# Performance work log

Hardware: AMD Instinct MI355X
Metric: run time of the kernel (lower is better)

## Reference

```python
import jax, jax.numpy as jnp
import numpy as np

N_NODES = 100000


def setup_inputs() -> dict:
    key = jax.random.key(0)
    k1, k2, k3, k4, k5 = jax.random.split(key, 5)
    feature = jax.random.normal(k1, (N_NODES, 64), dtype=jnp.float32)
    src = jax.random.randint(k2, (1600000,), 0, N_NODES, dtype=jnp.int64)
    dst = jax.random.randint(k3, (1600000,), 0, N_NODES, dtype=jnp.int64)
    W = jax.random.normal(k4, (64, 64), dtype=jnp.float32) * 0.1  # [in_feats, out_feats]
    b = jax.random.normal(k5, (64,), dtype=jnp.float32) * 0.1
    return {"feature": feature, "src": src, "dst": dst, "W": W, "b": b}


def reference(feature, src, dst, W, b):
    # message: m_e = h[src_e]; reduce: mean over mailbox per dst node.
    msgs = feature[src]                                   # [E, d] gather
    summed = jax.ops.segment_sum(msgs, dst, num_segments=N_NODES)  # [N, d]
    ones = jnp.ones((dst.shape[0],), dtype=feature.dtype)
    deg = jax.ops.segment_sum(ones, dst, num_segments=N_NODES)    # [N]
    mean = summed / jnp.maximum(deg, 1.0)[:, None]
    # DGL: nodes with no incoming messages keep their original feature
    h = jnp.where((deg > 0)[:, None], mean, feature)
    # apply_nodes: ReLU(W h + b)
    out = jax.nn.relu(h @ W + b)
    return out
```

## Files before the change

### kernel.cpp

```cpp
#include <hip/hip_runtime.h>
#include <hip/hip_bf16.h>

#define D 64
#define LOGB 7
#define BNODES 128
#define GRP6 32
#define CH6 1024
#define SUBN 32
#define CHUNK 1024
#define TN 64

__device__ __forceinline__ float blo(unsigned u) { return __uint_as_float(u << 16); }
__device__ __forceinline__ float bhi(unsigned u) { return __uint_as_float(u & 0xffff0000u); }
__device__ __forceinline__ ushort f2bfr(float x) {
    __hip_bfloat16 hb = __float2bfloat16(x);
    return *reinterpret_cast<ushort*>(&hb);
}


__global__ __launch_bounds__(256) void k_transform5(
    const float* __restrict__ feat, const float* __restrict__ W,
    ushort* __restrict__ g, int n_nodes,
    const int* __restrict__ dst, int n_edges,
    int* __restrict__ bcnt, int nbkt, int hb)
{
    __shared__ float ft[D][TN];
    __shared__ float Ws[D][D];
    __shared__ int sc[1024];

    int t = threadIdx.x;
    int n0 = blockIdx.x * TN;

    if (blockIdx.x == 0 && t < 64) g[(size_t)n_nodes * D + t] = 0;

    {
        const float4* W4 = (const float4*)W;
        float4* Ws4 = (float4*)&Ws[0][0];
        #pragma unroll
        for (int i = 0; i < 4; ++i) Ws4[t + i * 256] = W4[t + i * 256];
    }
    {
        const float4* f4 = (const float4*)feat;
        #pragma unroll
        for (int it = 0; it < 4; ++it) {
            int i = it * 256 + t;
            int r = i >> 4, c = i & 15;
            int node = n0 + r;
            float4 v = (node < n_nodes) ? f4[(size_t)node * 16 + c]
                                        : make_float4(0.f, 0.f, 0.f, 0.f);
            ft[4 * c + 0][r] = v.x;
            ft[4 * c + 1][r] = v.y;
            ft[4 * c + 2][r] = v.z;
            ft[4 * c + 3][r] = v.w;
        }
    }
    __syncthreads();

    int nq = t >> 4, cq = t & 15;
    int n4 = nq * 4, c4 = cq * 4;

    float4 a0 = make_float4(0.f, 0.f, 0.f, 0.f);
    float4 a1 = a0, a2 = a0, a3 = a0;

    #pragma unroll 16
    for (int k = 0; k < D; ++k) {
        float4 fv = *reinterpret_cast<const float4*>(&ft[k][n4]);
        float4 wv = *reinterpret_cast<const float4*>(&Ws[k][c4]);
        a0.x = fmaf(fv.x, wv.x, a0.x); a0.y = fmaf(fv.x, wv.y, a0.y);
        a0.z = fmaf(fv.x, wv.z, a0.z); a0.w = fmaf(fv.x, wv.w, a0.w);
        a1.x = fmaf(fv.y, wv.x, a1.x); a1.y = fmaf(fv.y, wv.y, a1.y);
        a1.z = fmaf(fv.y, wv.z, a1.z); a1.w = fmaf(fv.y, wv.w, a1.w);
        a2.x = fmaf(fv.z, wv.x, a2.x); a2.y = fmaf(fv.z, wv.y, a2.y);
        a2.z = fmaf(fv.z, wv.z, a2.z); a2.w = fmaf(fv.z, wv.w, a2.w);
        a3.x = fmaf(fv.w, wv.x, a3.x); a3.y = fmaf(fv.w, wv.y, a3.y);
        a3.z = fmaf(fv.w, wv.z, a3.z); a3.w = fmaf(fv.w, wv.w, a3.w);
    }

    float4 accs[4] = {a0, a1, a2, a3};
    #pragma unroll
    for (int i = 0; i < 4; ++i) {
        int node = n0 + n4 + i;
        if (node < n_nodes) {
            ushort4 o;
            o.x = f2bfr(accs[i].x);
            o.y = f2bfr(accs[i].y);
            o.z = f2bfr(accs[i].z);
            o.w = f2bfr(accs[i].w);
            *reinterpret_cast<ushort4*>(g + (size_t)node * D + c4) = o;
        }
    }

    if (blockIdx.x < (unsigned)hb) {
        for (int i = t; i < 1024; i += 256) sc[i] = 0;
        __syncthreads();
        int n4e = n_edges >> 2;
        const int4* d4 = (const int4*)dst;
        int base = blockIdx.x * 4096;
        #pragma unroll
        for (int k2 = 0; k2 < 16; ++k2) {
            int i = base + k2 * 256 + t;
            if (i < n4e) {
                int4 d = d4[i];
                atomicAdd(&sc[d.x >> LOGB], 1);
                atomicAdd(&sc[d.y >> LOGB], 1);
                atomicAdd(&sc[d.z >> LOGB], 1);
                atomicAdd(&sc[d.w >> LOGB], 1);
            }
        }
        if (blockIdx.x == 0 && t == 0)
            for (int e = n4e << 2; e < n_edges; ++e)
                atomicAdd(&bcnt[dst[e] >> LOGB], 1);
        __syncthreads();
        for (int i = t; i < nbkt; i += 256) {
            int c = sc[i];
            if (c) atomicAdd(&bcnt[i], c);
        }
    }
}


__global__ __launch_bounds__(256) void k_bin_count(
    const int* __restrict__ dst, int* __restrict__ cnt, int n_edges, int nbkt)
{
    __shared__ int sc[1024];
    int t = threadIdx.x;
    for (int i = t; i < 1024; i += 256) sc[i] = 0;
    __syncthreads();
    int n4 = n_edges >> 2;
    const int4* d4 = (const int4*)dst;
    int stride = gridDim.x * 256;
    for (int i = blockIdx.x * 256 + t; i < n4; i += stride) {
        int4 d = d4[i];
        atomicAdd(&sc[d.x >> LOGB], 1);
        atomicAdd(&sc[d.y >> LOGB], 1);
        atomicAdd(&sc[d.z >> LOGB], 1);
        atomicAdd(&sc[d.w >> LOGB], 1);
    }
    if (blockIdx.x == 0 && t == 0)
        for (int e = n4 << 2; e < n_edges; ++e) atomicAdd(&cnt[dst[e] >> LOGB], 1);
    __syncthreads();
    for (int i = t; i < nbkt; i += 256) {
        int c = sc[i];
        if (c) atomicAdd(&cnt[i], c);
    }
}

__global__ __launch_bounds__(1024) void k_bin_scan(
    const int* __restrict__ cnt, int* __restrict__ base,
    int* __restrict__ cursor, int nbkt)
{
    int t = threadIdx.x;
    int v = (t < nbkt) ? cnt[t] : 0;
    int lane = t & 63;
    int incl = v;
    #pragma unroll
    for (int o = 1; o < 64; o <<= 1) {
        int u = __shfl_up(incl, o, 64);
        if (lane >= o) incl += u;
    }
    __shared__ int wtot[16];
    if (lane == 63) wtot[t >> 6] = incl;
    __syncthreads();
    int wpre = 0;
    int w = t >> 6;
    for (int i = 0; i < w; ++i) wpre += wtot[i];
    int excl = wpre + incl - v;
    if (t < nbkt) { base[t] = excl; cursor[t] = excl; }
    if (t == nbkt - 1) base[nbkt] = excl + v;
}

__global__ __launch_bounds__(256) void k_bin_scatter(
    const int* __restrict__ src, const int* __restrict__ dst,
    int* __restrict__ cursor, unsigned* __restrict__ packed,
    int n_edges, int sbits)
{
    __shared__ int s_cnt[1024];
    __shared__ int s_base[1024];
    __shared__ int s_gb[1024];
    __shared__ int wtot[4];
    __shared__ unsigned s_stage[4096];
    __shared__ int s_addr[4096];

    int t = threadIdx.x;
    int chbase = blockIdx.x * 4096;
    int count = n_edges - chbase;
    if (count > 4096) count = 4096;

    for (int i = t; i < 1024; i += 256) s_cnt[i] = 0;
    __syncthreads();

    #pragma unroll
    for (int k = 0; k < 16; ++k) {
        int i = t + k * 256;
        if (i < count) atomicAdd(&s_cnt[dst[chbase + i] >> LOGB], 1);
    }
    __syncthreads();

    int b4 = t * 4;
    int v0 = s_cnt[b4], v1 = s_cnt[b4 + 1], v2 = s_cnt[b4 + 2], v3 = s_cnt[b4 + 3];
    int ssum = v0 + v1 + v2 + v3;
    int lane = t & 63;
    int incl = ssum;
    #pragma unroll
    for (int o = 1; o < 64; o <<= 1) {
        int u = __shfl_up(incl, o, 64);
        if (lane >= o) incl += u;
    }
    if (lane == 63) wtot[t >> 6] = incl;
    __syncthreads();
    int wpre = 0;
    int w = t >> 6;
    for (int i = 0; i < w; ++i) wpre += wtot[i];
    int excl = wpre + incl - ssum;
    s_base[b4]     = excl;
    s_base[b4 + 1] = excl + v0;
    s_base[b4 + 2] = excl + v0 + v1;
    s_base[b4 + 3] = excl + v0 + v1 + v2;
    __syncthreads();

    for (int i = t; i < 1024; i += 256) {
        int c = s_cnt[i];
        s_gb[i] = c ? atomicAdd(&cursor[i], c) : 0;
    }
    __syncthreads();
    for (int i = t; i < 1024; i += 256) s_cnt[i] = s_base[i];
    __syncthreads();

    #pragma unroll
    for (int k = 0; k < 16; ++k) {
        int i = t + k * 256;
        if (i < count) {
            int e = chbase + i;
            int d = dst[e];
            int s = src[e];
            int bkt = d >> LOGB;
            int pos = atomicAdd(&s_cnt[bkt], 1);
            s_stage[pos] = ((unsigned)(d & (BNODES - 1)) << sbits) | (unsigned)s;
            s_addr[pos]  = s_gb[bkt] + (pos - s_base[bkt]);
        }
    }
    __syncthreads();

    #pragma unroll
    for (int k = 0; k < 16; ++k) {
        int i = t + k * 256;
        if (i < count) packed[s_addr[i]] = s_stage[i];
    }
}


__global__ __launch_bounds__(256) void k_sort128(
    const unsigned* __restrict__ packed,
    const int* __restrict__ bbase,
    int* __restrict__ csr2,
    int* __restrict__ noff,
    int n_nodes, int sbits)
{
    __shared__ int s_cnt[BNODES];
    __shared__ int s_off[BNODES + 1];

    int t = threadIdx.x;
    int b = blockIdx.x;
    int gb = bbase[b], cnt = bbase[b + 1] - gb;

    if (t < BNODES) s_cnt[t] = 0;
    __syncthreads();
    for (int i = t; i < cnt; i += 256)
        atomicAdd(&s_cnt[packed[gb + i] >> sbits], 1);
    __syncthreads();

    if (t < 64) {
        int v0 = s_cnt[2 * t], v1 = s_cnt[2 * t + 1];
        int s = v0 + v1, incl = s;
        #pragma unroll
        for (int o = 1; o < 64; o <<= 1) {
            int u = __shfl_up(incl, o, 64);
            if (t >= o) incl += u;
        }
        int excl = incl - s;
        s_off[2 * t] = excl;
        s_off[2 * t + 1] = excl + v0;
        if (t == 63) s_off[BNODES] = incl;
    }
    __syncthreads();

    if (t <= BNODES) {
        int node = b * BNODES + t;
        if (node <= n_nodes) noff[node] = gb + s_off[t];
    }
    if (t < BNODES) s_cnt[t] = s_off[t];
    __syncthreads();

    unsigned smask = (1u << sbits) - 1u;
    for (int i = t; i < cnt; i += 256) {
        unsigned v = packed[gb + i];
        int pos = atomicAdd(&s_cnt[v >> sbits], 1);
        csr2[gb + pos] = (int)(v & smask);
    }
}


__global__ __launch_bounds__(256) void k_bucket6(
    const ushort* __restrict__ g,
    const float* __restrict__ bias,
    const int* __restrict__ noff,
    const int* __restrict__ csr2,
    float* __restrict__ out, int n_nodes)
{
    __shared__ int s_src[CH6];
    __shared__ int s_noff[GRP6 + 1];

    int t = threadIdx.x;
    int n0 = blockIdx.x * GRP6;
    if (t <= GRP6) {
        int node = n0 + t;
        s_noff[t] = noff[node > n_nodes ? n_nodes : node];
    }
    __syncthreads();

    int lane = t & 63, wid = t >> 6;
    int q = lane >> 4;
    int m = lane & 15;
    const ushort* gm = g + 4 * m;

    float4 acc[8];
    #pragma unroll
    for (int k = 0; k < 8; ++k) acc[k] = make_float4(0.f, 0.f, 0.f, 0.f);

    int beg = s_noff[0], end = s_noff[GRP6];
    for (int cb = beg; cb < end; cb += CH6) {
        int ce = cb + CH6 < end ? cb + CH6 : end;
        __syncthreads();
        for (int i = cb + t; i < ce; i += 256) s_src[i - cb] = csr2[i];
        __syncthreads();

        #pragma unroll
        for (int k = 0; k < 8; ++k) {
            int r = wid * 8 + k;
            int lo = s_noff[r], hi = s_noff[r + 1];
            if (lo < cb) lo = cb;
            if (hi > ce) hi = ce;
            float4 a = acc[k];
            for (int i = lo; i < hi; i += 16) {
                int i0 = i + q, i1 = i0 + 4, i2 = i0 + 8, i3 = i0 + 12;
                int s0 = (i0 < hi) ? s_src[i0 - cb] : n_nodes;
                int s1 = (i1 < hi) ? s_src[i1 - cb] : n_nodes;
                int s2 = (i2 < hi) ? s_src[i2 - cb] : n_nodes;
                int s3 = (i3 < hi) ? s_src[i3 - cb] : n_nodes;
                uint2 u0 = *reinterpret_cast<const uint2*>(gm + (size_t)s0 * D);
                uint2 u1 = *reinterpret_cast<const uint2*>(gm + (size_t)s1 * D);
                uint2 u2 = *reinterpret_cast<const uint2*>(gm + (size_t)s2 * D);
                uint2 u3 = *reinterpret_cast<const uint2*>(gm + (size_t)s3 * D);
                a.x += blo(u0.x); a.y += bhi(u0.x); a.z += blo(u0.y); a.w += bhi(u0.y);
                a.x += blo(u1.x); a.y += bhi(u1.x); a.z += blo(u1.y); a.w += bhi(u1.y);
                a.x += blo(u2.x); a.y += bhi(u2.x); a.z += blo(u2.y); a.w += bhi(u2.y);
                a.x += blo(u3.x); a.y += bhi(u3.x); a.z += blo(u3.y); a.w += bhi(u3.y);
            }
            acc[k] = a;
        }
    }

    float4 bj = *reinterpret_cast<const float4*>(bias + 4 * m);
    #pragma unroll
    for (int k = 0; k < 8; ++k) {
        float4 v = acc[k];
        v.x += __shfl_xor(v.x, 16, 64);
        v.y += __shfl_xor(v.y, 16, 64);
        v.z += __shfl_xor(v.z, 16, 64);
        v.w += __shfl_xor(v.w, 16, 64);
        v.x += __shfl_xor(v.x, 32, 64);
        v.y += __shfl_xor(v.y, 32, 64);
        v.z += __shfl_xor(v.z, 32, 64);
        v.w += __shfl_xor(v.w, 32, 64);
        if ((k & 3) == q) {
            int r = wid * 8 + k;
            int node = n0 + r;
            if (node < n_nodes) {
                int dgt = s_noff[r + 1] - s_noff[r];
                float4 res;
                if (dgt > 0) {
                    float inv = 1.0f / (float)dgt;
                    res = make_float4(v.x * inv, v.y * inv, v.z * inv, v.w * inv);
                } else {
                    uint2 u = *reinterpret_cast<const uint2*>(gm + (size_t)node * D);
                    res = make_float4(blo(u.x), bhi(u.x), blo(u.y), bhi(u.y));
                }
                res.x = fmaxf(res.x + bj.x, 0.0f);
                res.y = fmaxf(res.y + bj.y, 0.0f);
                res.z = fmaxf(res.z + bj.z, 0.0f);
                res.w = fmaxf(res.w + bj.w, 0.0f);
                *reinterpret_cast<float4*>(out + (size_t)node * D + 4 * m) = res;
            }
        }
    }
}


__global__ __launch_bounds__(256) void k_bucket4(
    const ushort* __restrict__ g,
    const float* __restrict__ bias,
    const int* __restrict__ base,
    const unsigned* __restrict__ packed,
    float* __restrict__ out,
    int n_nodes, int sbits)
{
    __shared__ unsigned s_raw[CHUNK];
    __shared__ unsigned s_rec[CHUNK];
    __shared__ int s_cnt[SUBN];
    __shared__ int s_off[SUBN + 1];

    int t = threadIdx.x;
    int lane = t & 63;
    int wid  = t >> 6;
    int q = lane >> 4;
    int m = lane & 15;
    int bkt = blockIdx.x >> 2;
    int sub = blockIdx.x & 3;
    int gb = base[bkt], ge = base[bkt + 1];
    unsigned smask = (1u << sbits) - 1u;
    const ushort* gm = g + 4 * m;

    float4 acc[8];
    int degv[8];
    #pragma unroll
    for (int k = 0; k < 8; ++k) {
        acc[k] = make_float4(0.f, 0.f, 0.f, 0.f);
        degv[k] = 0;
    }

    for (int cb = gb; cb < ge; cb += CHUNK) {
        int cnt = ge - cb;
        if (cnt > CHUNK) cnt = CHUNK;
        __syncthreads();
        if (t < SUBN) s_cnt[t] = 0;
        for (int i = t; i < cnt; i += 256) s_raw[i] = packed[cb + i];
        __syncthreads();
        for (int i = t; i < cnt; i += 256) {
            unsigned key = s_raw[i] >> sbits;
            if ((int)(key >> 5) == sub) atomicAdd(&s_cnt[key & 31], 1);
        }
        __syncthreads();
        if (t < 32) {
            int v = s_cnt[t];
            int incl = v;
            #pragma unroll
            for (int o = 1; o < 32; o <<= 1) {
                int u = __shfl_up(incl, o, 64);
                if (t >= o) incl += u;
            }
            int excl = incl - v;
            s_off[t] = excl;
            s_cnt[t] = excl;
            if (t == 31) s_off[32] = incl;
        }
        __syncthreads();
        for (int i = t; i < cnt; i += 256) {
            unsigned v = s_raw[i];
            unsigned key = v >> sbits;
            if ((int)(key >> 5) == sub) {
                int pos = atomicAdd(&s_cnt[key & 31], 1);
                s_rec[pos] = v;
            }
        }
        __syncthreads();
        #pragma unroll
        for (int k = 0; k < 8; ++k) {
            int r = wid * 8 + k;
            int beg = s_off[r], end = s_off[r + 1];
            float4 a = acc[k];
            for (int i = beg; i < end; i += 16) {
                int i0 = i + q, i1 = i0 + 4, i2 = i0 + 8, i3 = i0 + 12;
                bool p0 = i0 < end, p1 = i1 < end, p2 = i2 < end, p3 = i3 < end;
                unsigned r0 = s_rec[p0 ? i0 : beg];
                unsigned r1 = s_rec[p1 ? i1 : beg];
                unsigned r2 = s_rec[p2 ? i2 : beg];
                unsigned r3 = s_rec[p3 ? i3 : beg];
                int s0 = (int)(r0 & smask), s1 = (int)(r1 & smask);
                int s2 = (int)(r2 & smask), s3 = (int)(r3 & smask);
                uint2 u0 = *reinterpret_cast<const uint2*>(gm + (size_t)s0 * D);
                uint2 u1 = *reinterpret_cast<const uint2*>(gm + (size_t)s1 * D);
                uint2 u2 = *reinterpret_cast<const uint2*>(gm + (size_t)s2 * D);
                uint2 u3 = *reinterpret_cast<const uint2*>(gm + (size_t)s3 * D);
                a.x += p0 ? blo(u0.x) : 0.0f;  a.y += p0 ? bhi(u0.x) : 0.0f;
                a.z += p0 ? blo(u0.y) : 0.0f;  a.w += p0 ? bhi(u0.y) : 0.0f;
                a.x += p1 ? blo(u1.x) : 0.0f;  a.y += p1 ? bhi(u1.x) : 0.0f;
                a.z += p1 ? blo(u1.y) : 0.0f;  a.w += p1 ? bhi(u1.y) : 0.0f;
                a.x += p2 ? blo(u2.x) : 0.0f;  a.y += p2 ? bhi(u2.x) : 0.0f;
                a.z += p2 ? blo(u2.y) : 0.0f;  a.w += p2 ? bhi(u2.y) : 0.0f;
                a.x += p3 ? blo(u3.x) : 0.0f;  a.y += p3 ? bhi(u3.x) : 0.0f;
                a.z += p3 ? blo(u3.y) : 0.0f;  a.w += p3 ? bhi(u3.y) : 0.0f;
            }
            acc[k] = a;
            degv[k] += end - beg;
        }
    }

    float4 bj = *reinterpret_cast<const float4*>(bias + 4 * m);
    int n0 = (bkt << LOGB) + sub * SUBN;
    #pragma unroll
    for (int k = 0; k < 8; ++k) {
        float4 v = acc[k];
        v.x += __shfl_xor(v.x, 16, 64);
        v.y += __shfl_xor(v.y, 16, 64);
        v.z += __shfl_xor(v.z, 16, 64);
        v.w += __shfl_xor(v.w, 16, 64);
        v.x += __shfl_xor(v.x, 32, 64);
        v.y += __shfl_xor(v.y, 32, 64);
        v.z += __shfl_xor(v.z, 32, 64);
        v.w += __shfl_xor(v.w, 32, 64);
        if ((k & 3) == q) {
            int node = n0 + wid * 8 + k;
            if (node < n_nodes) {
                int dgt = degv[k];
                float4 res;
                if (dgt > 0) {
                    float inv = 1.0f / (float)dgt;
                    res = make_float4(v.x * inv, v.y * inv, v.z * inv, v.w * inv);
                } else {
                    uint2 u = *reinterpret_cast<const uint2*>(gm + (size_t)node * D);
                    res = make_float4(blo(u.x), bhi(u.x), blo(u.y), bhi(u.y));
                }
                res.x = fmaxf(res.x + bj.x, 0.0f);
                res.y = fmaxf(res.y + bj.y, 0.0f);
                res.z = fmaxf(res.z + bj.z, 0.0f);
                res.w = fmaxf(res.w + bj.w, 0.0f);
                *reinterpret_cast<float4*>(out + (size_t)node * D + 4 * m) = res;
            }
        }
    }
}


extern "C" void kernel_launch(void* const* d_in, const int* in_sizes, int n_in,
                              void* d_out, int out_size, void* d_ws, size_t ws_size,
                              hipStream_t stream)
{
    const float* feat = (const float*)d_in[0];
    const int*   src  = (const int*)d_in[1];
    const int*   dst  = (const int*)d_in[2];
    const float* W    = (const float*)d_in[3];
    const float* b    = (const float*)d_in[4];
    float* out = (float*)d_out;

    int n_nodes = in_sizes[0] / D;
    int n_edges = in_sizes[1];
    int nbkt = (n_nodes + BNODES - 1) >> LOGB;

    int sbits = 1;
    while ((1 << sbits) < n_nodes && sbits < 25) sbits++;

    size_t base_off   = 0;
    size_t cnt_off    = (((size_t)(nbkt + 1) * 4) + 63) & ~(size_t)63;
    size_t cursor_off = (cnt_off + (size_t)nbkt * 4 + 63) & ~(size_t)63;
    size_t noff_off   = (cursor_off + (size_t)nbkt * 4 + 63) & ~(size_t)63;
    size_t packed_off = (noff_off + ((size_t)n_nodes + 1) * 4 + 63) & ~(size_t)63;
    size_t csr2_off   = (packed_off + (size_t)n_edges * 4 + 63) & ~(size_t)63;
    size_t g_off      = (csr2_off + (size_t)n_edges * 4 + 63) & ~(size_t)63;
    size_t need_new   = g_off + ((size_t)n_nodes + 1) * D * 2;

    size_t o_packed_off = noff_off;
    size_t o_g_off      = (o_packed_off + (size_t)n_edges * 4 + 63) & ~(size_t)63;
    size_t need_old     = o_g_off + ((size_t)n_nodes + 1) * D * 2;

    bool common_ok = (nbkt <= 1024) && (sbits + LOGB <= 32) &&
                     ((1 << sbits) >= n_nodes);
    char* ws = (char*)d_ws;
    int tblk = (n_nodes + TN - 1) / TN;
    int nblk = (n_edges + 4095) / 4096;
    int hb = ((n_edges >> 2) + 4095) / 4096;
    bool fuse_hist = (hb <= tblk);

    if (common_ok && ws_size >= need_new) {
        int* bbase   = (int*)(ws + base_off);
        int* bcnt    = (int*)(ws + cnt_off);
        int* bcursor = (int*)(ws + cursor_off);
        int* noff    = (int*)(ws + noff_off);
        unsigned* packed = (unsigned*)(ws + packed_off);
        int* csr2    = (int*)(ws + csr2_off);
        ushort* g    = (ushort*)(ws + g_off);

        hipMemsetAsync(bcnt, 0, (size_t)nbkt * 4, stream);
        k_transform5<<<tblk, 256, 0, stream>>>(feat, W, g, n_nodes, dst, n_edges,
                                               bcnt, nbkt, fuse_hist ? hb : 0);
        if (!fuse_hist)
            k_bin_count<<<512, 256, 0, stream>>>(dst, bcnt, n_edges, nbkt);
        k_bin_scan<<<1, 1024, 0, stream>>>(bcnt, bbase, bcursor, nbkt);
        k_bin_scatter<<<nblk, 256, 0, stream>>>(src, dst, bcursor, packed,
                                                n_edges, sbits);
        k_sort128<<<nbkt, 256, 0, stream>>>(packed, bbase, csr2, noff,
                                            n_nodes, sbits);
        int ngrp6 = (n_nodes + GRP6 - 1) / GRP6;
        k_bucket6<<<ngrp6, 256, 0, stream>>>(g, b, noff, csr2, out, n_nodes);
    } else if (common_ok && ws_size >= need_old) {
        int* bbase   = (int*)(ws + base_off);
        int* bcnt    = (int*)(ws + cnt_off);
        int* bcursor = (int*)(ws + cursor_off);
        unsigned* packed = (unsigned*)(ws + o_packed_off);
        ushort* g    = (ushort*)(ws + o_g_off);

        hipMemsetAsync(bcnt, 0, (size_t)nbkt * 4, stream);
        k_transform5<<<tblk, 256, 0, stream>>>(feat, W, g, n_nodes, dst, n_edges,
                                               bcnt, nbkt, fuse_hist ? hb : 0);
        if (!fuse_hist)
            k_bin_count<<<512, 256, 0, stream>>>(dst, bcnt, n_edges, nbkt);
        k_bin_scan<<<1, 1024, 0, stream>>>(bcnt, bbase, bcursor, nbkt);
        k_bin_scatter<<<nblk, 256, 0, stream>>>(src, dst, bcursor, packed,
                                                n_edges, sbits);
        k_bucket4<<<nbkt * 4, 256, 0, stream>>>(g, b, bbase, packed, out,
                                                n_nodes, sbits);
    }
}
```

Baseline: 101.1 us.

## Move feature transform into scatter kernel and run histogram standalone

The histogram is split out of the transform kernel into a standalone k_hist launch with 256 blocks. The dense feature transform (h@W to bf16) now shares one launch with the bin scatter, with block ranges picking which path runs, so the GEMM blocks overlap the scatter's atomic-heavy work. The unused fallback k_bucket4 path is dropped, and the function returns early if workspace is too small. Using shared memory as a union of both paths' layouts raises per-block LDS use to about 45 KB, which may lower occupancy for the transform blocks.

```diff
diff --git a/kernel.cpp b/kernel.cpp
--- a/kernel.cpp
+++ b/kernel.cpp
@@ -6,8 +6,6 @@
 #define BNODES 128
 #define GRP6 32
 #define CH6 1024
-#define SUBN 32
-#define CHUNK 1024
 #define TN 64
 
 __device__ __forceinline__ float blo(unsigned u) { return __uint_as_float(u << 16); }
@@ -18,108 +16,7 @@
 }
 
 
-__global__ __launch_bounds__(256) void k_transform5(
-    const float* __restrict__ feat, const float* __restrict__ W,
-    ushort* __restrict__ g, int n_nodes,
-    const int* __restrict__ dst, int n_edges,
-    int* __restrict__ bcnt, int nbkt, int hb)
-{
-    __shared__ float ft[D][TN];
-    __shared__ float Ws[D][D];
-    __shared__ int sc[1024];
-
-    int t = threadIdx.x;
-    int n0 = blockIdx.x * TN;
-
-    if (blockIdx.x == 0 && t < 64) g[(size_t)n_nodes * D + t] = 0;
-
-    {
-        const float4* W4 = (const float4*)W;
-        float4* Ws4 = (float4*)&Ws[0][0];
-        #pragma unroll
-        for (int i = 0; i < 4; ++i) Ws4[t + i * 256] = W4[t + i * 256];
-    }
-    {
-        const float4* f4 = (const float4*)feat;
-        #pragma unroll
-        for (int it = 0; it < 4; ++it) {
-            int i = it * 256 + t;
-            int r = i >> 4, c = i & 15;
-            int node = n0 + r;
-            float4 v = (node < n_nodes) ? f4[(size_t)node * 16 + c]
-                                        : make_float4(0.f, 0.f, 0.f, 0.f);
-            ft[4 * c + 0][r] = v.x;
-            ft[4 * c + 1][r] = v.y;
-            ft[4 * c + 2][r] = v.z;
-            ft[4 * c + 3][r] = v.w;
-        }
-    }
-    __syncthreads();
-
-    int nq = t >> 4, cq = t & 15;
-    int n4 = nq * 4, c4 = cq * 4;
-
-    float4 a0 = make_float4(0.f, 0.f, 0.f, 0.f);
-    float4 a1 = a0, a2 = a0, a3 = a0;
-
-    #pragma unroll 16
-    for (int k = 0; k < D; ++k) {
-        float4 fv = *reinterpret_cast<const float4*>(&ft[k][n4]);
-        float4 wv = *reinterpret_cast<const float4*>(&Ws[k][c4]);
-        a0.x = fmaf(fv.x, wv.x, a0.x); a0.y = fmaf(fv.x, wv.y, a0.y);
-        a0.z = fmaf(fv.x, wv.z, a0.z); a0.w = fmaf(fv.x, wv.w, a0.w);
-        a1.x = fmaf(fv.y, wv.x, a1.x); a1.y = fmaf(fv.y, wv.y, a1.y);
-        a1.z = fmaf(fv.y, wv.z, a1.z); a1.w = fmaf(fv.y, wv.w, a1.w);
-        a2.x = fmaf(fv.z, wv.x, a2.x); a2.y = fmaf(fv.z, wv.y, a2.y);
-        a2.z = fmaf(fv.z, wv.z, a2.z); a2.w = fmaf(fv.z, wv.w, a2.w);
-        a3.x = fmaf(fv.w, wv.x, a3.x); a3.y = fmaf(fv.w, wv.y, a3.y);
-        a3.z = fmaf(fv.w, wv.z, a3.z); a3.w = fmaf(fv.w, wv.w, a3.w);
-    }
-
-    float4 accs[4] = {a0, a1, a2, a3};
-    #pragma unroll
-    for (int i = 0; i < 4; ++i) {
-        int node = n0 + n4 + i;
-        if (node < n_nodes) {
-            ushort4 o;
-            o.x = f2bfr(accs[i].x);
-            o.y = f2bfr(accs[i].y);
-            o.z = f2bfr(accs[i].z);
-            o.w = f2bfr(accs[i].w);
-            *reinterpret_cast<ushort4*>(g + (size_t)node * D + c4) = o;
-        }
-    }
-
-    if (blockIdx.x < (unsigned)hb) {
-        for (int i = t; i < 1024; i += 256) sc[i] = 0;
-        __syncthreads();
-        int n4e = n_edges >> 2;
-        const int4* d4 = (const int4*)dst;
-        int base = blockIdx.x * 4096;
-        #pragma unroll
-        for (int k2 = 0; k2 < 16; ++k2) {
-            int i = base + k2 * 256 + t;
-            if (i < n4e) {
-                int4 d = d4[i];
-                atomicAdd(&sc[d.x >> LOGB], 1);
-                atomicAdd(&sc[d.y >> LOGB], 1);
-                atomicAdd(&sc[d.z >> LOGB], 1);
-                atomicAdd(&sc[d.w >> LOGB], 1);
-            }
-        }
-        if (blockIdx.x == 0 && t == 0)
-            for (int e = n4e << 2; e < n_edges; ++e)
-                atomicAdd(&bcnt[dst[e] >> LOGB], 1);
-        __syncthreads();
-        for (int i = t; i < nbkt; i += 256) {
-            int c = sc[i];
-            if (c) atomicAdd(&bcnt[i], c);
-        }
-    }
-}
-
-
-__global__ __launch_bounds__(256) void k_bin_count(
+__global__ __launch_bounds__(256) void k_hist(
     const int* __restrict__ dst, int* __restrict__ cnt, int n_edges, int nbkt)
 {
     __shared__ int sc[1024];
@@ -145,6 +42,7 @@
     }
 }
 
+
 __global__ __launch_bounds__(1024) void k_bin_scan(
     const int* __restrict__ cnt, int* __restrict__ base,
     int* __restrict__ cursor, int nbkt)
@@ -169,82 +67,154 @@
     if (t == nbkt - 1) base[nbkt] = excl + v;
 }
 
-__global__ __launch_bounds__(256) void k_bin_scatter(
+
+__global__ __launch_bounds__(256) void k_fused(
     const int* __restrict__ src, const int* __restrict__ dst,
     int* __restrict__ cursor, unsigned* __restrict__ packed,
-    int n_edges, int sbits)
-{
-    __shared__ int s_cnt[1024];
-    __shared__ int s_base[1024];
-    __shared__ int s_gb[1024];
-    __shared__ int wtot[4];
-    __shared__ unsigned s_stage[4096];
-    __shared__ int s_addr[4096];
-
+    int n_edges, int sbits, int nblk,
+    const float* __restrict__ feat, const float* __restrict__ W,
+    ushort* __restrict__ g, int n_nodes)
+{
+    __shared__ __align__(16) char smem[45072];
     int t = threadIdx.x;
-    int chbase = blockIdx.x * 4096;
-    int count = n_edges - chbase;
-    if (count > 4096) count = 4096;
-
-    for (int i = t; i < 1024; i += 256) s_cnt[i] = 0;
-    __syncthreads();
-
-    #pragma unroll
-    for (int k = 0; k < 16; ++k) {
-        int i = t + k * 256;
-        if (i < count) atomicAdd(&s_cnt[dst[chbase + i] >> LOGB], 1);
-    }
-    __syncthreads();
-
-    int b4 = t * 4;
-    int v0 = s_cnt[b4], v1 = s_cnt[b4 + 1], v2 = s_cnt[b4 + 2], v3 = s_cnt[b4 + 3];
-    int ssum = v0 + v1 + v2 + v3;
-    int lane = t & 63;
-    int incl = ssum;
-    #pragma unroll
-    for (int o = 1; o < 64; o <<= 1) {
-        int u = __shfl_up(incl, o, 64);
-        if (lane >= o) incl += u;
-    }
-    if (lane == 63) wtot[t >> 6] = incl;
-    __syncthreads();
-    int wpre = 0;
-    int w = t >> 6;
-    for (int i = 0; i < w; ++i) wpre += wtot[i];
-    int excl = wpre + incl - ssum;
-    s_base[b4]     = excl;
-    s_base[b4 + 1] = excl + v0;
-    s_base[b4 + 2] = excl + v0 + v1;
-    s_base[b4 + 3] = excl + v0 + v1 + v2;
-    __syncthreads();
-
-    for (int i = t; i < 1024; i += 256) {
-        int c = s_cnt[i];
-        s_gb[i] = c ? atomicAdd(&cursor[i], c) : 0;
-    }
-    __syncthreads();
-    for (int i = t; i < 1024; i += 256) s_cnt[i] = s_base[i];
-    __syncthreads();
-
-    #pragma unroll
-    for (int k = 0; k < 16; ++k) {
-        int i = t + k * 256;
-        if (i < count) {
-            int e = chbase + i;
-            int d = dst[e];
-            int s = src[e];
-            int bkt = d >> LOGB;
-            int pos = atomicAdd(&s_cnt[bkt], 1);
-            s_stage[pos] = ((unsigned)(d & (BNODES - 1)) << sbits) | (unsigned)s;
-            s_addr[pos]  = s_gb[bkt] + (pos - s_base[bkt]);
-        }
-    }
-    __syncthreads();
-
-    #pragma unroll
-    for (int k = 0; k < 16; ++k) {
-        int i = t + k * 256;
-        if (i < count) packed[s_addr[i]] = s_stage[i];
+
+    if ((int)blockIdx.x < nblk) {
+        int* s_cnt  = (int*)smem;
+        int* s_base = (int*)(smem + 4096);
+        int* s_gb   = (int*)(smem + 8192);
+        int* wtot   = (int*)(smem + 12288);
+        unsigned* s_stage = (unsigned*)(smem + 12304);
+        int* s_addr = (int*)(smem + 28688);
+
+        int chbase = blockIdx.x * 4096;
+        int count = n_edges - chbase;
+        if (count > 4096) count = 4096;
+
+        for (int i = t; i < 1024; i += 256) s_cnt[i] = 0;
+        __syncthreads();
+
+        #pragma unroll
+        for (int k = 0; k < 16; ++k) {
+            int i = t + k * 256;
+            if (i < count) atomicAdd(&s_cnt[dst[chbase + i] >> LOGB], 1);
+        }
+        __syncthreads();
+
+        int b4 = t * 4;
+        int v0 = s_cnt[b4], v1 = s_cnt[b4 + 1], v2 = s_cnt[b4 + 2], v3 = s_cnt[b4 + 3];
+        int ssum = v0 + v1 + v2 + v3;
+        int lane = t & 63;
+        int incl = ssum;
+        #pragma unroll
+        for (int o = 1; o < 64; o <<= 1) {
+            int u = __shfl_up(incl, o, 64);
+            if (lane >= o) incl += u;
+        }
+        if (lane == 63) wtot[t >> 6] = incl;
+        __syncthreads();
+        int wpre = 0;
+        int w = t >> 6;
+        for (int i = 0; i < w; ++i) wpre += wtot[i];
+        int excl = wpre + incl - ssum;
+        s_base[b4]     = excl;
+        s_base[b4 + 1] = excl + v0;
+        s_base[b4 + 2] = excl + v0 + v1;
+        s_base[b4 + 3] = excl + v0 + v1 + v2;
+        __syncthreads();
+
+        for (int i = t; i < 1024; i += 256) {
+            int c = s_cnt[i];
+            s_gb[i] = c ? atomicAdd(&cursor[i], c) : 0;
+        }
+        __syncthreads();
+        for (int i = t; i < 1024; i += 256) s_cnt[i] = s_base[i];
+        __syncthreads();
+
+        #pragma unroll
+        for (int k = 0; k < 16; ++k) {
+            int i = t + k * 256;
+            if (i < count) {
+                int e = chbase + i;
+                int d = dst[e];
+                int s = src[e];
+                int bkt = d >> LOGB;
+                int pos = atomicAdd(&s_cnt[bkt], 1);
+                s_stage[pos] = ((unsigned)(d & (BNODES - 1)) << sbits) | (unsigned)s;
+                s_addr[pos]  = s_gb[bkt] + (pos - s_base[bkt]);
+            }
+        }
+        __syncthreads();
+
+        #pragma unroll
+        for (int k = 0; k < 16; ++k) {
+            int i = t + k * 256;
+            if (i < count) packed[s_addr[i]] = s_stage[i];
+        }
+    } else {
+        float* ft = (float*)smem;
+        float* Ws = (float*)(smem + 16384);
+
+        int bid = blockIdx.x - nblk;
+        int n0 = bid * TN;
+
+        if (bid == 0 && t < 64) g[(size_t)n_nodes * D + t] = 0;
+
+        {
+            const float4* W4 = (const float4*)W;
+            float4* Ws4 = (float4*)Ws;
+            #pragma unroll
+            for (int i = 0; i < 4; ++i) Ws4[t + i * 256] = W4[t + i * 256];
+        }
+        {
+            const float4* f4 = (const float4*)feat;
+            #pragma unroll
+            for (int it = 0; it < 4; ++it) {
+                int i = it * 256 + t;
+                int r = i >> 4, c = i & 15;
+                int node = n0 + r;
+                float4 v = (node < n_nodes) ? f4[(size_t)node * 16 + c]
+                                            : make_float4(0.f, 0.f, 0.f, 0.f);
+                ft[(4 * c + 0) * TN + r] = v.x;
+                ft[(4 * c + 1) * TN + r] = v.y;
+                ft[(4 * c + 2) * TN + r] = v.z;
+                ft[(4 * c + 3) * TN + r] = v.w;
+            }
+        }
+        __syncthreads();
+
+        int nq = t >> 4, cq = t & 15;
+        int n4 = nq * 4, c4 = cq * 4;
+
+        float4 a0 = make_float4(0.f, 0.f, 0.f, 0.f);
+        float4 a1 = a0, a2 = a0, a3 = a0;
+
+        #pragma unroll 16
+        for (int k = 0; k < D; ++k) {
+            float4 fv = *reinterpret_cast<const float4*>(&ft[k * TN + n4]);
+            float4 wv = *reinterpret_cast<const float4*>(&Ws[k * D + c4]);
+            a0.x = fmaf(fv.x, wv.x, a0.x); a0.y = fmaf(fv.x, wv.y, a0.y);
+            a0.z = fmaf(fv.x, wv.z, a0.z); a0.w = fmaf(fv.x, wv.w, a0.w);
+            a1.x = fmaf(fv.y, wv.x, a1.x); a1.y = fmaf(fv.y, wv.y, a1.y);
+            a1.z = fmaf(fv.y, wv.z, a1.z); a1.w = fmaf(fv.y, wv.w, a1.w);
+            a2.x = fmaf(fv.z, wv.x, a2.x); a2.y = fmaf(fv.z, wv.y, a2.y);
+            a2.z = fmaf(fv.z, wv.z, a2.z); a2.w = fmaf(fv.z, wv.w, a2.w);
+            a3.x = fmaf(fv.w, wv.x, a3.x); a3.y = fmaf(fv.w, wv.y, a3.y);
+            a3.z = fmaf(fv.w, wv.z, a3.z); a3.w = fmaf(fv.w, wv.w, a3.w);
+        }
+
+        float4 accs[4] = {a0, a1, a2, a3};
+        #pragma unroll
+        for (int i = 0; i < 4; ++i) {
+            int node = n0 + n4 + i;
+            if (node < n_nodes) {
+                ushort4 o;
+                o.x = f2bfr(accs[i].x);
+                o.y = f2bfr(accs[i].y);
+                o.z = f2bfr(accs[i].z);
+                o.w = f2bfr(accs[i].w);
+                *reinterpret_cast<ushort4*>(g + (size_t)node * D + c4) = o;
+            }
+        }
     }
 }
 
@@ -396,141 +366,6 @@
 }
 
 
-__global__ __launch_bounds__(256) void k_bucket4(
-    const ushort* __restrict__ g,
-    const float* __restrict__ bias,
-    const int* __restrict__ base,
-    const unsigned* __restrict__ packed,
-    float* __restrict__ out,
-    int n_nodes, int sbits)
-{
-    __shared__ unsigned s_raw[CHUNK];
-    __shared__ unsigned s_rec[CHUNK];
-    __shared__ int s_cnt[SUBN];
-    __shared__ int s_off[SUBN + 1];
-
-    int t = threadIdx.x;
-    int lane = t & 63;
-    int wid  = t >> 6;
-    int q = lane >> 4;
-    int m = lane & 15;
-    int bkt = blockIdx.x >> 2;
-    int sub = blockIdx.x & 3;
-    int gb = base[bkt], ge = base[bkt + 1];
-    unsigned smask = (1u << sbits) - 1u;
-    const ushort* gm = g + 4 * m;
-
-    float4 acc[8];
-    int degv[8];
-    #pragma unroll
-    for (int k = 0; k < 8; ++k) {
-        acc[k] = make_float4(0.f, 0.f, 0.f, 0.f);
-        degv[k] = 0;
-    }
-
-    for (int cb = gb; cb < ge; cb += CHUNK) {
-        int cnt = ge - cb;
-        if (cnt > CHUNK) cnt = CHUNK;
-        __syncthreads();
-        if (t < SUBN) s_cnt[t] = 0;
-        for (int i = t; i < cnt; i += 256) s_raw[i] = packed[cb + i];
-        __syncthreads();
-        for (int i = t; i < cnt; i += 256) {
-            unsigned key = s_raw[i] >> sbits;
-            if ((int)(key >> 5) == sub) atomicAdd(&s_cnt[key & 31], 1);
-        }
-        __syncthreads();
-        if (t < 32) {
-            int v = s_cnt[t];
-            int incl = v;
-            #pragma unroll
-            for (int o = 1; o < 32; o <<= 1) {
-                int u = __shfl_up(incl, o, 64);
-                if (t >= o) incl += u;
-            }
-            int excl = incl - v;
-            s_off[t] = excl;
-            s_cnt[t] = excl;
-            if (t == 31) s_off[32] = incl;
-        }
-        __syncthreads();
-        for (int i = t; i < cnt; i += 256) {
-            unsigned v = s_raw[i];
-            unsigned key = v >> sbits;
-            if ((int)(key >> 5) == sub) {
-                int pos = atomicAdd(&s_cnt[key & 31], 1);
-                s_rec[pos] = v;
-            }
-        }
-        __syncthreads();
-        #pragma unroll
-        for (int k = 0; k < 8; ++k) {
-            int r = wid * 8 + k;
-            int beg = s_off[r], end = s_off[r + 1];
-            float4 a = acc[k];
-            for (int i = beg; i < end; i += 16) {
-                int i0 = i + q, i1 = i0 + 4, i2 = i0 + 8, i3 = i0 + 12;
-                bool p0 = i0 < end, p1 = i1 < end, p2 = i2 < end, p3 = i3 < end;
-                unsigned r0 = s_rec[p0 ? i0 : beg];
-                unsigned r1 = s_rec[p1 ? i1 : beg];
-                unsigned r2 = s_rec[p2 ? i2 : beg];
-                unsigned r3 = s_rec[p3 ? i3 : beg];
-                int s0 = (int)(r0 & smask), s1 = (int)(r1 & smask);
-                int s2 = (int)(r2 & smask), s3 = (int)(r3 & smask);
-                uint2 u0 = *reinterpret_cast<const uint2*>(gm + (size_t)s0 * D);
-                uint2 u1 = *reinterpret_cast<const uint2*>(gm + (size_t)s1 * D);
-                uint2 u2 = *reinterpret_cast<const uint2*>(gm + (size_t)s2 * D);
-                uint2 u3 = *reinterpret_cast<const uint2*>(gm + (size_t)s3 * D);
-                a.x += p0 ? blo(u0.x) : 0.0f;  a.y += p0 ? bhi(u0.x) : 0.0f;
-                a.z += p0 ? blo(u0.y) : 0.0f;  a.w += p0 ? bhi(u0.y) : 0.0f;
-                a.x += p1 ? blo(u1.x) : 0.0f;  a.y += p1 ? bhi(u1.x) : 0.0f;
-                a.z += p1 ? blo(u1.y) : 0.0f;  a.w += p1 ? bhi(u1.y) : 0.0f;
-                a.x += p2 ? blo(u2.x) : 0.0f;  a.y += p2 ? bhi(u2.x) : 0.0f;
-                a.z += p2 ? blo(u2.y) : 0.0f;  a.w += p2 ? bhi(u2.y) : 0.0f;
-                a.x += p3 ? blo(u3.x) : 0.0f;  a.y += p3 ? bhi(u3.x) : 0.0f;
-                a.z += p3 ? blo(u3.y) : 0.0f;  a.w += p3 ? bhi(u3.y) : 0.0f;
-            }
-            acc[k] = a;
-            degv[k] += end - beg;
-        }
-    }
-
-    float4 bj = *reinterpret_cast<const float4*>(bias + 4 * m);
-    int n0 = (bkt << LOGB) + sub * SUBN;
-    #pragma unroll
-    for (int k = 0; k < 8; ++k) {
-        float4 v = acc[k];
-        v.x += __shfl_xor(v.x, 16, 64);
-        v.y += __shfl_xor(v.y, 16, 64);
-        v.z += __shfl_xor(v.z, 16, 64);
-        v.w += __shfl_xor(v.w, 16, 64);
-        v.x += __shfl_xor(v.x, 32, 64);
-        v.y += __shfl_xor(v.y, 32, 64);
-        v.z += __shfl_xor(v.z, 32, 64);
-        v.w += __shfl_xor(v.w, 32, 64);
-        if ((k & 3) == q) {
-            int node = n0 + wid * 8 + k;
-            if (node < n_nodes) {
-                int dgt = degv[k];
-                float4 res;
-                if (dgt > 0) {
-                    float inv = 1.0f / (float)dgt;
-                    res = make_float4(v.x * inv, v.y * inv, v.z * inv, v.w * inv);
-                } else {
-                    uint2 u = *reinterpret_cast<const uint2*>(gm + (size_t)node * D);
-                    res = make_float4(blo(u.x), bhi(u.x), blo(u.y), bhi(u.y));
-                }
-                res.x = fmaxf(res.x + bj.x, 0.0f);
-                res.y = fmaxf(res.y + bj.y, 0.0f);
-                res.z = fmaxf(res.z + bj.z, 0.0f);
-                res.w = fmaxf(res.w + bj.w, 0.0f);
-                *reinterpret_cast<float4*>(out + (size_t)node * D + 4 * m) = res;
-            }
-        }
-    }
-}
-
-
 extern "C" void kernel_launch(void* const* d_in, const int* in_sizes, int n_in,
                               void* d_out, int out_size, void* d_ws, size_t ws_size,
                               hipStream_t stream)
@@ -556,57 +391,32 @@
     size_t packed_off = (noff_off + ((size_t)n_nodes + 1) * 4 + 63) & ~(size_t)63;
     size_t csr2_off   = (packed_off + (size_t)n_edges * 4 + 63) & ~(size_t)63;
     size_t g_off      = (csr2_off + (size_t)n_edges * 4 + 63) & ~(size_t)63;
-    size_t need_new   = g_off + ((size_t)n_nodes + 1) * D * 2;
-
-    size_t o_packed_off = noff_off;
-    size_t o_g_off      = (o_packed_off + (size_t)n_edges * 4 + 63) & ~(size_t)63;
-    size_t need_old     = o_g_off + ((size_t)n_nodes + 1) * D * 2;
-
-    bool common_ok = (nbkt <= 1024) && (sbits + LOGB <= 32) &&
-                     ((1 << sbits) >= n_nodes);
+    size_t need       = g_off + ((size_t)n_nodes + 1) * D * 2;
+
+    bool ok = (ws_size >= need) && (nbkt <= 1024) && (sbits + LOGB <= 32) &&
+              ((1 << sbits) >= n_nodes);
+    if (!ok) return;
+
     char* ws = (char*)d_ws;
+    int* bbase   = (int*)(ws + base_off);
+    int* bcnt    = (int*)(ws + cnt_off);
+    int* bcursor = (int*)(ws + cursor_off);
+    int* noff    = (int*)(ws + noff_off);
+    unsigned* packed = (unsigned*)(ws + packed_off);
+    int* csr2    = (int*)(ws + csr2_off);
+    ushort* g    = (ushort*)(ws + g_off);
+
     int tblk = (n_nodes + TN - 1) / TN;
     int nblk = (n_edges + 4095) / 4096;
-    int hb = ((n_edges >> 2) + 4095) / 4096;
-    bool fuse_hist = (hb <= tblk);
-
-    if (common_ok && ws_size >= need_new) {
-        int* bbase   = (int*)(ws + base_off);
-        int* bcnt    = (int*)(ws + cnt_off);
-        int* bcursor = (int*)(ws + cursor_off);
-        int* noff    = (int*)(ws + noff_off);
-        unsigned* packed = (unsigned*)(ws + packed_off);
-        int* csr2    = (int*)(ws + csr2_off);
-        ushort* g    = (ushort*)(ws + g_off);
-
-        hipMemsetAsync(bcnt, 0, (size_t)nbkt * 4, stream);
-        k_transform5<<<tblk, 256, 0, stream>>>(feat, W, g, n_nodes, dst, n_edges,
-                                               bcnt, nbkt, fuse_hist ? hb : 0);
-        if (!fuse_hist)
-            k_bin_count<<<512, 256, 0, stream>>>(dst, bcnt, n_edges, nbkt);
-        k_bin_scan<<<1, 1024, 0, stream>>>(bcnt, bbase, bcursor, nbkt);
-        k_bin_scatter<<<nblk, 256, 0, stream>>>(src, dst, bcursor, packed,
-                                                n_edges, sbits);
-        k_sort128<<<nbkt, 256, 0, stream>>>(packed, bbase, csr2, noff,
-                                            n_nodes, sbits);
-        int ngrp6 = (n_nodes + GRP6 - 1) / GRP6;
-        k_bucket6<<<ngrp6, 256, 0, stream>>>(g, b, noff, csr2, out, n_nodes);
-    } else if (common_ok && ws_size >= need_old) {
-        int* bbase   = (int*)(ws + base_off);
-        int* bcnt    = (int*)(ws + cnt_off);
-        int* bcursor = (int*)(ws + cursor_off);
-        unsigned* packed = (unsigned*)(ws + o_packed_off);
-        ushort* g    = (ushort*)(ws + o_g_off);
-
-        hipMemsetAsync(bcnt, 0, (size_t)nbkt * 4, stream);
-        k_transform5<<<tblk, 256, 0, stream>>>(feat, W, g, n_nodes, dst, n_edges,
-                                               bcnt, nbkt, fuse_hist ? hb : 0);
-        if (!fuse_hist)
-            k_bin_count<<<512, 256, 0, stream>>>(dst, bcnt, n_edges, nbkt);
-        k_bin_scan<<<1, 1024, 0, stream>>>(bcnt, bbase, bcursor, nbkt);
-        k_bin_scatter<<<nblk, 256, 0, stream>>>(src, dst, bcursor, packed,
-                                                n_edges, sbits);
-        k_bucket4<<<nbkt * 4, 256, 0, stream>>>(g, b, bbase, packed, out,
-                                                n_nodes, sbits);
-    }
-}
+
+    hipMemsetAsync(bcnt, 0, (size_t)nbkt * 4, stream);
+    k_hist<<<256, 256, 0, stream>>>(dst, bcnt, n_edges, nbkt);
+    k_bin_scan<<<1, 1024, 0, stream>>>(bcnt, bbase, bcursor, nbkt);
+    k_fused<<<nblk + tblk, 256, 0, stream>>>(src, dst, bcursor, packed,
+                                             n_edges, sbits, nblk,
+                                             feat, W, g, n_nodes);
+    k_sort128<<<nbkt, 256, 0, stream>>>(packed, bbase, csr2, noff,
+                                        n_nodes, sbits);
+    int ngrp6 = (n_nodes + GRP6 - 1) / GRP6;
+    k_bucket6<<<ngrp6, 256, 0, stream>>>(g, b, noff, csr2, out, n_nodes);
+}
```

New measurement: 100.1 us. No clear change (-1.0%).
